# Performance work log

Measured on AMD Instinct MI355X. Metric: run time of the kernel, lower is better.

## Reference

```python
import jax, jax.numpy as jnp
import numpy as np

V, K, NB = 200000, 24, 10
P = K * 9  # pose-blendshape feature dim = 216
# Standard SMPL/STAR kinematic tree; root's parent set to itself (handled specially).
PARENTS = np.array([0, 0, 0, 0, 1, 2, 3, 4, 5, 6, 7, 8, 9, 9, 9, 12, 13, 14, 16, 17, 18, 19, 20, 21])


def setup_inputs() -> dict:
    key = jax.random.key(0)
    ks = jax.random.split(key, 7)
    return {
        "betas": jax.random.normal(ks[0], (NB,), dtype=jnp.float32),
        "pose": jax.random.normal(ks[1], (K * 3,), dtype=jnp.float32),
        "v_template": jax.random.normal(ks[2], (V, 3), dtype=jnp.float32),
        "shapedirs": jax.random.normal(ks[3], (V, 3, NB), dtype=jnp.float32) * 0.01,
        "posedirs": jax.random.normal(ks[4], (V, 3, P), dtype=jnp.float32) * 0.01,
        "J_regressor": jax.random.uniform(ks[5], (K, V), dtype=jnp.float32) / V,
        "weights": jax.random.uniform(ks[6], (V, K), dtype=jnp.float32),
    }


def _rodrigues(r):
    # r: (K,3) axis-angle -> (K,3,3) rotation matrices (matches torch version incl. +1e-12)
    theta = jnp.linalg.norm(r + 1e-12, axis=1, keepdims=True)  # (K,1)
    k = r / theta
    kx, ky, kz = k[:, 0], k[:, 1], k[:, 2]
    z = jnp.zeros_like(kx)
    Km = jnp.stack([z, -kz, ky, kz, z, -kx, -ky, kx, z], axis=1).reshape(-1, 3, 3)
    s = jnp.sin(theta)[:, :, None]
    c = jnp.cos(theta)[:, :, None]
    return jnp.eye(3, dtype=r.dtype) + s * Km + (1.0 - c) * (Km @ Km)


def reference(betas, pose, v_template, shapedirs, posedirs, J_regressor, weights):
    # shape blendshapes
    v_shaped = v_template + jnp.einsum('vci,i->vc', shapedirs, betas)  # (V,3)
    J = J_regressor @ v_shaped  # (K,3) joint locations in rest pose
    R = _rodrigues(pose.reshape(K, 3))  # (K,3,3)
    # pose blendshapes: features are (R - I) flattened over all K joints
    pose_feat = (R - jnp.eye(3, dtype=R.dtype)).reshape(-1)  # (K*9,)
    v_posed = v_shaped + jnp.einsum('vcp,p->vc', posedirs, pose_feat)
    # relative joint translations along the kinematic chain
    rel = J - J[PARENTS]
    rel = rel.at[0].set(J[0])
    # forward kinematics: A[j] = A[parent] @ [[R_j, rel_j],[0,1]]  (K=24, unrolled)
    A_rot = [R[0]]
    A_t = [rel[0]]
    for j in range(1, K):
        p = int(PARENTS[j])
        A_rot.append(A_rot[p] @ R[j])
        A_t.append(A_rot[p] @ rel[j] + A_t[p])
    rot = jnp.stack(A_rot)  # (K,3,3)
    # T[k] = A[k] @ inv(A_rest[k]); A_rest is pure translation by J[k], so
    # T_rot = rot, T_trans = A_t - rot @ J  (analytic inverse of translation)
    trans = jnp.stack(A_t) - jnp.einsum('kij,kj->ki', rot, J)  # (K,3)
    # LBS: blend transforms per vertex (avoids dense K x V x 4 intermediate)
    W_rot = jnp.einsum('vk,kij->vij', weights, rot)  # (V,3,3)
    W_t = weights @ trans  # (V,3)
    return jnp.einsum('vij,vj->vi', W_rot, v_posed) + W_t  # (V,3)
```

## Files before the change

kernel.cpp:

```cpp
#include <hip/hip_runtime.h>

#define NV 200000
#define NPAIR 100000
#define NK 24
#define NCH 64

#define PART_OFF 0
#define J_OFF    4608
#define ROT_OFF  4680
#define TR_OFF   4896
#define PF_OFF   4968

template <int CTRL>
__device__ __forceinline__ float dpp_add(float x) {
    int y = __builtin_amdgcn_update_dpp(0, __float_as_int(x), CTRL, 0xf, 0xf, true);
    return x + __int_as_float(y);
}

typedef float vfloat4 __attribute__((ext_vector_type(4)));
typedef float vfloat2 __attribute__((ext_vector_type(2)));

__device__ __forceinline__ float4 nt_load4(const float4* p) {
    vfloat4 r = __builtin_nontemporal_load((const vfloat4*)p);
    return make_float4(r.x, r.y, r.z, r.w);
}
__device__ __forceinline__ float2 nt_load2(const float2* p) {
    vfloat2 r = __builtin_nontemporal_load((const vfloat2*)p);
    return make_float2(r.x, r.y);
}
__device__ __forceinline__ float nt_load1(const float* p) {
    return __builtin_nontemporal_load(p);
}

__global__ __launch_bounds__(256) void kA(const float* __restrict__ vt,
                                          const float* __restrict__ sd,
                                          const float* __restrict__ betas,
                                          float* __restrict__ vs_out) {
    int v = blockIdx.x * 256 + threadIdx.x;
    if (v >= NV) return;
    float b[10];
#pragma unroll
    for (int i = 0; i < 10; i++) b[i] = betas[i];
    size_t v3 = 3 * (size_t)v;
    float acc0 = nt_load1(vt + v3), acc1 = nt_load1(vt + v3 + 1), acc2 = nt_load1(vt + v3 + 2);
    const float2* s2 = (const float2*)(sd) + (size_t)v * 15;
#pragma unroll
    for (int j = 0; j < 15; j++) {
        float2 s = nt_load2(s2 + j);
        const int e0 = 2 * j, e1 = 2 * j + 1;
        float p0 = s.x * b[e0 % 10];
        float p1 = s.y * b[e1 % 10];
        if (e0 / 10 == 0) acc0 += p0; else if (e0 / 10 == 1) acc1 += p0; else acc2 += p0;
        if (e1 / 10 == 0) acc0 += p1; else if (e1 / 10 == 1) acc1 += p1; else acc2 += p1;
    }
    vs_out[v3] = acc0; vs_out[v3 + 1] = acc1; vs_out[v3 + 2] = acc2;
}

__global__ __launch_bounds__(256) void kB(const float* __restrict__ jr,
                                          const float* __restrict__ vs,
                                          float* __restrict__ ws) {
    int k = blockIdx.x >> 6;
    int chunk = blockIdx.x & 63;
    const float* row = jr + (size_t)k * NV;
    float a0 = 0.f, a1 = 0.f, a2 = 0.f;
    for (int v = chunk * 256 + threadIdx.x; v < NV; v += NCH * 256) {
        float w = nt_load1(row + v);
        size_t v3 = 3 * (size_t)v;
        a0 = fmaf(w, vs[v3], a0);
        a1 = fmaf(w, vs[v3 + 1], a1);
        a2 = fmaf(w, vs[v3 + 2], a2);
    }
#pragma unroll
    for (int off = 32; off; off >>= 1) {
        a0 += __shfl_xor(a0, off, 64);
        a1 += __shfl_xor(a1, off, 64);
        a2 += __shfl_xor(a2, off, 64);
    }
    __shared__ float red[4][3];
    int lane = threadIdx.x & 63, wv = threadIdx.x >> 6;
    if (lane == 0) { red[wv][0] = a0; red[wv][1] = a1; red[wv][2] = a2; }
    __syncthreads();
    if (threadIdx.x < 3) {
        float s = red[0][threadIdx.x] + red[1][threadIdx.x] +
                  red[2][threadIdx.x] + red[3][threadIdx.x];
        ws[PART_OFF + blockIdx.x * 3 + threadIdx.x] = s;
    }
}

__global__ __launch_bounds__(64) void kC(const float* __restrict__ pose,
                                         float* __restrict__ ws) {
    __shared__ float Jl[72];
    __shared__ float Rl[24][9];
    __shared__ float Ar[24][9];
    __shared__ float At[24][3];
    int t = threadIdx.x;

    for (int idx = t; idx < 72; idx += 64) {
        int k = idx / 3, c = idx % 3;
        float s = 0.f;
#pragma unroll
        for (int ch = 0; ch < NCH; ch++) s += ws[PART_OFF + (k * NCH + ch) * 3 + c];
        Jl[idx] = s;
    }

    if (t < 24) {
        float rx = pose[3 * t], ry = pose[3 * t + 1], rz = pose[3 * t + 2];
        float tx = rx + 1e-12f, ty = ry + 1e-12f, tz = rz + 1e-12f;
        float th = sqrtf(tx * tx + ty * ty + tz * tz);
        float inv = 1.0f / th;
        float kx = rx * inv, ky = ry * inv, kz = rz * inv;
        float s = sinf(th), c = cosf(th), oc = 1.0f - c;
        float R00 = 1.f + oc * (-(ky * ky + kz * kz));
        float R01 = -s * kz + oc * kx * ky;
        float R02 =  s * ky + oc * kx * kz;
        float R10 =  s * kz + oc * kx * ky;
        float R11 = 1.f + oc * (-(kx * kx + kz * kz));
        float R12 = -s * kx + oc * ky * kz;
        float R20 = -s * ky + oc * kx * kz;
        float R21 =  s * kx + oc * ky * kz;
        float R22 = 1.f + oc * (-(kx * kx + ky * ky));
        Rl[t][0] = R00; Rl[t][1] = R01; Rl[t][2] = R02;
        Rl[t][3] = R10; Rl[t][4] = R11; Rl[t][5] = R12;
        Rl[t][6] = R20; Rl[t][7] = R21; Rl[t][8] = R22;
        float* pf = ws + PF_OFF + t * 9;
        pf[0] = R00 - 1.f; pf[1] = R01;       pf[2] = R02;
        pf[3] = R10;       pf[4] = R11 - 1.f; pf[5] = R12;
        pf[6] = R20;       pf[7] = R21;       pf[8] = R22 - 1.f;
    }
    __syncthreads();

    const int par[24] = {0,0,0,0,1,2,3,4,5,6,7,8,9,9,9,12,13,14,16,17,18,19,20,21};
    const int lvl[24] = {0,1,1,1,2,2,2,3,3,3,4,4,4,4,4,5,5,5,6,6,7,7,8,8};
    float rel0 = 0.f, rel1 = 0.f, rel2 = 0.f;
    int p = 0, myl = -1;
    if (t < 24) {
        p = par[t]; myl = lvl[t];
        if (t == 0) { rel0 = Jl[0]; rel1 = Jl[1]; rel2 = Jl[2]; }
        else {
            rel0 = Jl[3 * t]     - Jl[3 * p];
            rel1 = Jl[3 * t + 1] - Jl[3 * p + 1];
            rel2 = Jl[3 * t + 2] - Jl[3 * p + 2];
        }
    }
    for (int L = 0; L < 9; L++) {
        if (myl == L) {
            if (t == 0) {
#pragma unroll
                for (int e = 0; e < 9; e++) Ar[0][e] = Rl[0][e];
                At[0][0] = rel0; At[0][1] = rel1; At[0][2] = rel2;
            } else {
#pragma unroll
                for (int i = 0; i < 3; i++) {
                    float ai0 = Ar[p][i * 3], ai1 = Ar[p][i * 3 + 1], ai2 = Ar[p][i * 3 + 2];
#pragma unroll
                    for (int jj = 0; jj < 3; jj++) {
                        Ar[t][i * 3 + jj] = ai0 * Rl[t][jj] + ai1 * Rl[t][3 + jj] + ai2 * Rl[t][6 + jj];
                    }
                    At[t][i] = ai0 * rel0 + ai1 * rel1 + ai2 * rel2 + At[p][i];
                }
            }
        }
        __syncthreads();
    }
    if (t < 24) {
#pragma unroll
        for (int i = 0; i < 3; i++) {
            float tr = At[t][i] - (Ar[t][i * 3]     * Jl[3 * t] +
                                   Ar[t][i * 3 + 1] * Jl[3 * t + 1] +
                                   Ar[t][i * 3 + 2] * Jl[3 * t + 2]);
            ws[TR_OFF + t * 3 + i] = tr;
        }
#pragma unroll
        for (int e = 0; e < 9; e++) ws[ROT_OFF + t * 9 + e] = Ar[t][e];
    }
}

__global__ __launch_bounds__(256) void kD(const float* __restrict__ pd,
                                          const float* __restrict__ wts,
                                          const float* __restrict__ ws,
                                          float* __restrict__ out) {
    int t = threadIdx.x;
    int l = t & 63;

    const float4* pf4 = (const float4*)(ws + PF_OFF);
    float4 b0 = pf4[(l < 54) ? l      : l - 54];
    float4 b1 = pf4[(l < 44) ? l + 10 : l - 44];
    float4 b2 = pf4[(l < 34) ? l + 20 : l - 34];
    float4 b3 = pf4[(l < 24) ? l + 30 : l - 24];
    float4 b4 = pf4[(l < 14) ? l + 40 : l - 14];
    float4 b5 = pf4[(l <  4) ? l + 50 : 0];

    int h  = l >> 5;
    int kk = l & 31;
    float rr0=0,rr1=0,rr2=0,rr3=0,rr4=0,rr5=0,rr6=0,rr7=0,rr8=0;
    float tt0=0, tt1=0, tt2=0;
    if (kk < 24) {
        const float* r = ws + ROT_OFF + kk * 9;
        rr0=r[0]; rr1=r[1]; rr2=r[2]; rr3=r[3]; rr4=r[4];
        rr5=r[5]; rr6=r[6]; rr7=r[7]; rr8=r[8];
        const float* tr = ws + TR_OFF + kk * 3;
        tt0=tr[0]; tt1=tr[1]; tt2=tr[2];
    }

    int wid = (blockIdx.x << 2) + (t >> 6);
    int stride = gridDim.x << 2;
    for (int p = wid; p < NPAIR; p += stride) {
        const float4* base = (const float4*)(pd) + (size_t)p * 324;
        float4 A0 = nt_load4(base + l);
        float4 A1 = nt_load4(base + l + 64);
        float4 A2 = nt_load4(base + l + 128);
        float4 A3 = nt_load4(base + l + 192);
        float4 A4 = nt_load4(base + l + 256);
        float4 A5 = make_float4(0.f, 0.f, 0.f, 0.f);
        if (l < 4) A5 = nt_load4(base + l + 320);

        int vmy = 2 * p + h;
        const float* vsp = out + (size_t)vmy * 3;
        float vsx = vsp[0], vsy = vsp[1], vsz = vsp[2];
        float wk = (kk < 24) ? nt_load1(wts + (size_t)vmy * 24 + kk) : 0.f;

        float d0 = A0.x * b0.x + A0.y * b0.y + A0.z * b0.z + A0.w * b0.w;
        float d1 = A1.x * b1.x + A1.y * b1.y + A1.z * b1.z + A1.w * b1.w;
        float d2 = A2.x * b2.x + A2.y * b2.y + A2.z * b2.z + A2.w * b2.w;
        float d3 = A3.x * b3.x + A3.y * b3.y + A3.z * b3.z + A3.w * b3.w;
        float d4 = A4.x * b4.x + A4.y * b4.y + A4.z * b4.z + A4.w * b4.w;
        float d5 = A5.x * b5.x + A5.y * b5.y + A5.z * b5.z + A5.w * b5.w;

        float s0 = (l < 54) ? d0 : 0.f;
        float s1 = ((l < 54) ? 0.f : d0) + ((l < 44) ? d1 : 0.f);
        float s2 = ((l < 44) ? 0.f : d1) + ((l < 34) ? d2 : 0.f);
        float s3 = ((l < 34) ? 0.f : d2) + ((l < 24) ? d3 : 0.f);
        float s4 = ((l < 24) ? 0.f : d3) + ((l < 14) ? d4 : 0.f);
        float s5 = ((l < 14) ? 0.f : d4) + d5;

        s0 = dpp_add<0xB1>(s0); s1 = dpp_add<0xB1>(s1); s2 = dpp_add<0xB1>(s2);
        s3 = dpp_add<0xB1>(s3); s4 = dpp_add<0xB1>(s4); s5 = dpp_add<0xB1>(s5);
        s0 = dpp_add<0x4E>(s0); s1 = dpp_add<0x4E>(s1); s2 = dpp_add<0x4E>(s2);
        s3 = dpp_add<0x4E>(s3); s4 = dpp_add<0x4E>(s4); s5 = dpp_add<0x4E>(s5);
        s0 = dpp_add<0x141>(s0); s1 = dpp_add<0x141>(s1); s2 = dpp_add<0x141>(s2);
        s3 = dpp_add<0x141>(s3); s4 = dpp_add<0x141>(s4); s5 = dpp_add<0x141>(s5);
        s0 = dpp_add<0x140>(s0); s1 = dpp_add<0x140>(s1); s2 = dpp_add<0x140>(s2);
        s3 = dpp_add<0x140>(s3); s4 = dpp_add<0x140>(s4); s5 = dpp_add<0x140>(s5);
        s0 += __shfl_xor(s0, 16, 64); s1 += __shfl_xor(s1, 16, 64); s2 += __shfl_xor(s2, 16, 64);
        s3 += __shfl_xor(s3, 16, 64); s4 += __shfl_xor(s4, 16, 64); s5 += __shfl_xor(s5, 16, 64);
        s0 += __shfl_xor(s0, 32, 64); s1 += __shfl_xor(s1, 32, 64); s2 += __shfl_xor(s2, 32, 64);
        s3 += __shfl_xor(s3, 32, 64); s4 += __shfl_xor(s4, 32, 64); s5 += __shfl_xor(s5, 32, 64);

        float vpx = vsx + (h ? s3 : s0);
        float vpy = vsy + (h ? s4 : s1);
        float vpz = vsz + (h ? s5 : s2);

        float m0 = wk * (rr0 * vpx + rr1 * vpy + rr2 * vpz + tt0);
        float m1 = wk * (rr3 * vpx + rr4 * vpy + rr5 * vpz + tt1);
        float m2 = wk * (rr6 * vpx + rr7 * vpy + rr8 * vpz + tt2);

        m0 = dpp_add<0xB1>(m0); m1 = dpp_add<0xB1>(m1); m2 = dpp_add<0xB1>(m2);
        m0 = dpp_add<0x4E>(m0); m1 = dpp_add<0x4E>(m1); m2 = dpp_add<0x4E>(m2);
        m0 = dpp_add<0x141>(m0); m1 = dpp_add<0x141>(m1); m2 = dpp_add<0x141>(m2);
        m0 = dpp_add<0x140>(m0); m1 = dpp_add<0x140>(m1); m2 = dpp_add<0x140>(m2);
        m0 += __shfl_xor(m0, 16, 64); m1 += __shfl_xor(m1, 16, 64); m2 += __shfl_xor(m2, 16, 64);

        if (kk < 3) {
            out[(size_t)vmy * 3 + kk] = (kk == 0) ? m0 : (kk == 1) ? m1 : m2;
        }
    }
}

extern "C" void kernel_launch(void* const* d_in, const int* in_sizes, int n_in,
                              void* d_out, int out_size, void* d_ws, size_t ws_size,
                              hipStream_t stream) {
    const float* betas = (const float*)d_in[0];
    const float* pose  = (const float*)d_in[1];
    const float* vt    = (const float*)d_in[2];
    const float* sd    = (const float*)d_in[3];
    const float* pd    = (const float*)d_in[4];
    const float* jr    = (const float*)d_in[5];
    const float* wts   = (const float*)d_in[6];
    float* out = (float*)d_out;
    float* ws  = (float*)d_ws;

    kA<<<(NV + 255) / 256, 256, 0, stream>>>(vt, sd, betas, out);
    kB<<<NK * NCH, 256, 0, stream>>>(jr, out, ws);
    kC<<<1, 64, 0, stream>>>(pose, ws);
    kD<<<2048, 256, 0, stream>>>(pd, wts, ws, out);
}
```

Baseline: 120.8 us.

## Fuse four kernels into one cooperative persistent kernel with grid syncs

Replaces the four separate launches (shape blend, joint regression, kinematic chain, pose blend + skinning) with a single cooperative kernel that runs each phase in turn, separated by grid-wide syncs, and keeps the old launches as a fallback. The aim is to remove per-launch overhead and the gaps between kernels. In exchange it adds three grid barriers, caps the grid at what can be co-resident, and leaves the serial kinematic-chain phase on a single block while every other block waits.

```diff
diff --git a/kernel.cpp b/kernel.cpp
--- a/kernel.cpp
+++ b/kernel.cpp
@@ -1,12 +1,15 @@
 #include <hip/hip_runtime.h>
+#include <hip/hip_cooperative_groups.h>
+
+namespace cg = cooperative_groups;
 
 #define NV 200000
 #define NPAIR 100000
 #define NK 24
 #define NCH 64
+#define NTHREADS 256
 
 #define PART_OFF 0
-#define J_OFF    4608
 #define ROT_OFF  4680
 #define TR_OFF   4896
 #define PF_OFF   4968
@@ -32,17 +35,13 @@
     return __builtin_nontemporal_load(p);
 }
 
-__global__ __launch_bounds__(256) void kA(const float* __restrict__ vt,
-                                          const float* __restrict__ sd,
-                                          const float* __restrict__ betas,
-                                          float* __restrict__ vs_out) {
-    int v = blockIdx.x * 256 + threadIdx.x;
-    if (v >= NV) return;
+__device__ __forceinline__ void phaseA_body(int v, const float* vt, const float* sd,
+                                            const float* betas, float* out) {
     float b[10];
 #pragma unroll
     for (int i = 0; i < 10; i++) b[i] = betas[i];
     size_t v3 = 3 * (size_t)v;
-    float acc0 = nt_load1(vt + v3), acc1 = nt_load1(vt + v3 + 1), acc2 = nt_load1(vt + v3 + 2);
+    float a0 = nt_load1(vt + v3), a1 = nt_load1(vt + v3 + 1), a2 = nt_load1(vt + v3 + 2);
     const float2* s2 = (const float2*)(sd) + (size_t)v * 15;
 #pragma unroll
     for (int j = 0; j < 15; j++) {
@@ -50,59 +49,106 @@
         const int e0 = 2 * j, e1 = 2 * j + 1;
         float p0 = s.x * b[e0 % 10];
         float p1 = s.y * b[e1 % 10];
-        if (e0 / 10 == 0) acc0 += p0; else if (e0 / 10 == 1) acc1 += p0; else acc2 += p0;
-        if (e1 / 10 == 0) acc0 += p1; else if (e1 / 10 == 1) acc1 += p1; else acc2 += p1;
-    }
-    vs_out[v3] = acc0; vs_out[v3 + 1] = acc1; vs_out[v3 + 2] = acc2;
-}
-
-__global__ __launch_bounds__(256) void kB(const float* __restrict__ jr,
-                                          const float* __restrict__ vs,
-                                          float* __restrict__ ws) {
-    int k = blockIdx.x >> 6;
-    int chunk = blockIdx.x & 63;
-    const float* row = jr + (size_t)k * NV;
-    float a0 = 0.f, a1 = 0.f, a2 = 0.f;
-    for (int v = chunk * 256 + threadIdx.x; v < NV; v += NCH * 256) {
-        float w = nt_load1(row + v);
-        size_t v3 = 3 * (size_t)v;
-        a0 = fmaf(w, vs[v3], a0);
-        a1 = fmaf(w, vs[v3 + 1], a1);
-        a2 = fmaf(w, vs[v3 + 2], a2);
-    }
-#pragma unroll
-    for (int off = 32; off; off >>= 1) {
-        a0 += __shfl_xor(a0, off, 64);
-        a1 += __shfl_xor(a1, off, 64);
-        a2 += __shfl_xor(a2, off, 64);
-    }
-    __shared__ float red[4][3];
-    int lane = threadIdx.x & 63, wv = threadIdx.x >> 6;
-    if (lane == 0) { red[wv][0] = a0; red[wv][1] = a1; red[wv][2] = a2; }
-    __syncthreads();
-    if (threadIdx.x < 3) {
-        float s = red[0][threadIdx.x] + red[1][threadIdx.x] +
-                  red[2][threadIdx.x] + red[3][threadIdx.x];
-        ws[PART_OFF + blockIdx.x * 3 + threadIdx.x] = s;
-    }
-}
-
-__global__ __launch_bounds__(64) void kC(const float* __restrict__ pose,
-                                         float* __restrict__ ws) {
-    __shared__ float Jl[72];
-    __shared__ float Rl[24][9];
-    __shared__ float Ar[24][9];
-    __shared__ float At[24][3];
-    int t = threadIdx.x;
-
-    for (int idx = t; idx < 72; idx += 64) {
-        int k = idx / 3, c = idx % 3;
-        float s = 0.f;
-#pragma unroll
-        for (int ch = 0; ch < NCH; ch++) s += ws[PART_OFF + (k * NCH + ch) * 3 + c];
-        Jl[idx] = s;
-    }
-
+        if (e0 / 10 == 0) a0 += p0; else if (e0 / 10 == 1) a1 += p0; else a2 += p0;
+        if (e1 / 10 == 0) a0 += p1; else if (e1 / 10 == 1) a1 += p1; else a2 += p1;
+    }
+    out[v3] = a0; out[v3 + 1] = a1; out[v3 + 2] = a2;
+}
+
+struct DState {
+    float4 b0, b1, b2, b3, b4, b5;
+    float rr0, rr1, rr2, rr3, rr4, rr5, rr6, rr7, rr8, tt0, tt1, tt2;
+    int h, kk;
+};
+
+__device__ __forceinline__ void phaseD_init(DState& st, int l, const float* ws) {
+    const float4* pf4 = (const float4*)(ws + PF_OFF);
+    st.b0 = pf4[(l < 54) ? l      : l - 54];
+    st.b1 = pf4[(l < 44) ? l + 10 : l - 44];
+    st.b2 = pf4[(l < 34) ? l + 20 : l - 34];
+    st.b3 = pf4[(l < 24) ? l + 30 : l - 24];
+    st.b4 = pf4[(l < 14) ? l + 40 : l - 14];
+    st.b5 = pf4[(l <  4) ? l + 50 : 0];
+    st.h  = l >> 5;
+    st.kk = l & 31;
+    st.rr0=0; st.rr1=0; st.rr2=0; st.rr3=0; st.rr4=0; st.rr5=0;
+    st.rr6=0; st.rr7=0; st.rr8=0; st.tt0=0; st.tt1=0; st.tt2=0;
+    if (st.kk < 24) {
+        const float* r = ws + ROT_OFF + st.kk * 9;
+        st.rr0=r[0]; st.rr1=r[1]; st.rr2=r[2]; st.rr3=r[3]; st.rr4=r[4];
+        st.rr5=r[5]; st.rr6=r[6]; st.rr7=r[7]; st.rr8=r[8];
+        const float* tr = ws + TR_OFF + st.kk * 3;
+        st.tt0=tr[0]; st.tt1=tr[1]; st.tt2=tr[2];
+    }
+}
+
+__device__ __forceinline__ void phaseD_pair(const DState& st, int l, int p,
+                                            const float* pd, const float* wts,
+                                            float* out) {
+    const float4* base = (const float4*)(pd) + (size_t)p * 324;
+    float4 A0 = nt_load4(base + l);
+    float4 A1 = nt_load4(base + l + 64);
+    float4 A2 = nt_load4(base + l + 128);
+    float4 A3 = nt_load4(base + l + 192);
+    float4 A4 = nt_load4(base + l + 256);
+    float4 A5 = make_float4(0.f, 0.f, 0.f, 0.f);
+    if (l < 4) A5 = nt_load4(base + l + 320);
+
+    int vmy = 2 * p + st.h;
+    const float* vsp = out + (size_t)vmy * 3;
+    float vsx = vsp[0], vsy = vsp[1], vsz = vsp[2];
+    float wk = (st.kk < 24) ? nt_load1(wts + (size_t)vmy * 24 + st.kk) : 0.f;
+
+    float d0 = A0.x * st.b0.x + A0.y * st.b0.y + A0.z * st.b0.z + A0.w * st.b0.w;
+    float d1 = A1.x * st.b1.x + A1.y * st.b1.y + A1.z * st.b1.z + A1.w * st.b1.w;
+    float d2 = A2.x * st.b2.x + A2.y * st.b2.y + A2.z * st.b2.z + A2.w * st.b2.w;
+    float d3 = A3.x * st.b3.x + A3.y * st.b3.y + A3.z * st.b3.z + A3.w * st.b3.w;
+    float d4 = A4.x * st.b4.x + A4.y * st.b4.y + A4.z * st.b4.z + A4.w * st.b4.w;
+    float d5 = A5.x * st.b5.x + A5.y * st.b5.y + A5.z * st.b5.z + A5.w * st.b5.w;
+
+    float s0 = (l < 54) ? d0 : 0.f;
+    float s1 = ((l < 54) ? 0.f : d0) + ((l < 44) ? d1 : 0.f);
+    float s2 = ((l < 44) ? 0.f : d1) + ((l < 34) ? d2 : 0.f);
+    float s3 = ((l < 34) ? 0.f : d2) + ((l < 24) ? d3 : 0.f);
+    float s4 = ((l < 24) ? 0.f : d3) + ((l < 14) ? d4 : 0.f);
+    float s5 = ((l < 14) ? 0.f : d4) + d5;
+
+    s0 = dpp_add<0xB1>(s0); s1 = dpp_add<0xB1>(s1); s2 = dpp_add<0xB1>(s2);
+    s3 = dpp_add<0xB1>(s3); s4 = dpp_add<0xB1>(s4); s5 = dpp_add<0xB1>(s5);
+    s0 = dpp_add<0x4E>(s0); s1 = dpp_add<0x4E>(s1); s2 = dpp_add<0x4E>(s2);
+    s3 = dpp_add<0x4E>(s3); s4 = dpp_add<0x4E>(s4); s5 = dpp_add<0x4E>(s5);
+    s0 = dpp_add<0x141>(s0); s1 = dpp_add<0x141>(s1); s2 = dpp_add<0x141>(s2);
+    s3 = dpp_add<0x141>(s3); s4 = dpp_add<0x141>(s4); s5 = dpp_add<0x141>(s5);
+    s0 = dpp_add<0x140>(s0); s1 = dpp_add<0x140>(s1); s2 = dpp_add<0x140>(s2);
+    s3 = dpp_add<0x140>(s3); s4 = dpp_add<0x140>(s4); s5 = dpp_add<0x140>(s5);
+    s0 += __shfl_xor(s0, 16, 64); s1 += __shfl_xor(s1, 16, 64); s2 += __shfl_xor(s2, 16, 64);
+    s3 += __shfl_xor(s3, 16, 64); s4 += __shfl_xor(s4, 16, 64); s5 += __shfl_xor(s5, 16, 64);
+    s0 += __shfl_xor(s0, 32, 64); s1 += __shfl_xor(s1, 32, 64); s2 += __shfl_xor(s2, 32, 64);
+    s3 += __shfl_xor(s3, 32, 64); s4 += __shfl_xor(s4, 32, 64); s5 += __shfl_xor(s5, 32, 64);
+
+    float vpx = vsx + (st.h ? s3 : s0);
+    float vpy = vsy + (st.h ? s4 : s1);
+    float vpz = vsz + (st.h ? s5 : s2);
+
+    float m0 = wk * (st.rr0 * vpx + st.rr1 * vpy + st.rr2 * vpz + st.tt0);
+    float m1 = wk * (st.rr3 * vpx + st.rr4 * vpy + st.rr5 * vpz + st.tt1);
+    float m2 = wk * (st.rr6 * vpx + st.rr7 * vpy + st.rr8 * vpz + st.tt2);
+
+    m0 = dpp_add<0xB1>(m0); m1 = dpp_add<0xB1>(m1); m2 = dpp_add<0xB1>(m2);
+    m0 = dpp_add<0x4E>(m0); m1 = dpp_add<0x4E>(m1); m2 = dpp_add<0x4E>(m2);
+    m0 = dpp_add<0x141>(m0); m1 = dpp_add<0x141>(m1); m2 = dpp_add<0x141>(m2);
+    m0 = dpp_add<0x140>(m0); m1 = dpp_add<0x140>(m1); m2 = dpp_add<0x140>(m2);
+    m0 += __shfl_xor(m0, 16, 64); m1 += __shfl_xor(m1, 16, 64); m2 += __shfl_xor(m2, 16, 64);
+
+    if (st.kk < 3) {
+        out[(size_t)vmy * 3 + st.kk] = (st.kk == 0) ? m0 : (st.kk == 1) ? m1 : m2;
+    }
+}
+
+__device__ __forceinline__ void rodrigues_and_chain(int t, const float* pose,
+                                                    float* ws,
+                                                    float Jl[72], float Rl[24][9],
+                                                    float Ar[24][9], float At[24][3]) {
     if (t < 24) {
         float rx = pose[3 * t], ry = pose[3 * t + 1], rz = pose[3 * t + 2];
         float tx = rx + 1e-12f, ty = ry + 1e-12f, tz = rz + 1e-12f;
@@ -175,95 +221,153 @@
     }
 }
 
+__global__ __launch_bounds__(NTHREADS, 4) void mega(const float* __restrict__ betas,
+                                                    const float* __restrict__ pose,
+                                                    const float* __restrict__ vt,
+                                                    const float* __restrict__ sd,
+                                                    const float* __restrict__ pd,
+                                                    const float* __restrict__ jr,
+                                                    const float* __restrict__ wts,
+                                                    float* __restrict__ out,
+                                                    float* __restrict__ ws) {
+    cg::grid_group grid = cg::this_grid();
+    const int tid = threadIdx.x;
+    const int bid = blockIdx.x;
+    const int nb  = gridDim.x;
+    const int l = tid & 63;
+    const int wv = tid >> 6;
+
+    __shared__ float red[4][3];
+    __shared__ float Jl[72];
+    __shared__ float Rl[24][9];
+    __shared__ float Ar[24][9];
+    __shared__ float At[24][3];
+
+    for (int v = bid * NTHREADS + tid; v < NV; v += nb * NTHREADS)
+        phaseA_body(v, vt, sd, betas, out);
+    grid.sync();
+
+    for (int unit = bid; unit < NK * NCH; unit += nb) {
+        int k = unit >> 6;
+        int chunk = unit & 63;
+        const float* row = jr + (size_t)k * NV;
+        float a0 = 0.f, a1 = 0.f, a2 = 0.f;
+        for (int v = chunk * 256 + tid; v < NV; v += NCH * 256) {
+            float w = nt_load1(row + v);
+            size_t v3 = 3 * (size_t)v;
+            a0 = fmaf(w, out[v3], a0);
+            a1 = fmaf(w, out[v3 + 1], a1);
+            a2 = fmaf(w, out[v3 + 2], a2);
+        }
+#pragma unroll
+        for (int off = 32; off; off >>= 1) {
+            a0 += __shfl_xor(a0, off, 64);
+            a1 += __shfl_xor(a1, off, 64);
+            a2 += __shfl_xor(a2, off, 64);
+        }
+        if (l == 0) { red[wv][0] = a0; red[wv][1] = a1; red[wv][2] = a2; }
+        __syncthreads();
+        if (tid < 3) {
+            float s = red[0][tid] + red[1][tid] + red[2][tid] + red[3][tid];
+            ws[PART_OFF + unit * 3 + tid] = s;
+        }
+        __syncthreads();
+    }
+    grid.sync();
+
+    if (bid == 0) {
+        for (int idx = tid; idx < 72; idx += NTHREADS) {
+            int k = idx / 3, c = idx % 3;
+            float s = 0.f;
+#pragma unroll
+            for (int ch = 0; ch < NCH; ch++) s += ws[PART_OFF + (k * NCH + ch) * 3 + c];
+            Jl[idx] = s;
+        }
+        __syncthreads();
+        rodrigues_and_chain(tid, pose, ws, Jl, Rl, Ar, At);
+    }
+    grid.sync();
+
+    {
+        DState st;
+        phaseD_init(st, l, ws);
+        int wid = (bid << 2) + wv;
+        int stride = nb << 2;
+        for (int p = wid; p < NPAIR; p += stride)
+            phaseD_pair(st, l, p, pd, wts, out);
+    }
+}
+
+__global__ __launch_bounds__(256) void kA(const float* __restrict__ vt,
+                                          const float* __restrict__ sd,
+                                          const float* __restrict__ betas,
+                                          float* __restrict__ vs_out) {
+    int v = blockIdx.x * 256 + threadIdx.x;
+    if (v >= NV) return;
+    phaseA_body(v, vt, sd, betas, vs_out);
+}
+
+__global__ __launch_bounds__(256) void kB(const float* __restrict__ jr,
+                                          const float* __restrict__ vs,
+                                          float* __restrict__ ws) {
+    int k = blockIdx.x >> 6;
+    int chunk = blockIdx.x & 63;
+    const float* row = jr + (size_t)k * NV;
+    float a0 = 0.f, a1 = 0.f, a2 = 0.f;
+    for (int v = chunk * 256 + threadIdx.x; v < NV; v += NCH * 256) {
+        float w = nt_load1(row + v);
+        size_t v3 = 3 * (size_t)v;
+        a0 = fmaf(w, vs[v3], a0);
+        a1 = fmaf(w, vs[v3 + 1], a1);
+        a2 = fmaf(w, vs[v3 + 2], a2);
+    }
+#pragma unroll
+    for (int off = 32; off; off >>= 1) {
+        a0 += __shfl_xor(a0, off, 64);
+        a1 += __shfl_xor(a1, off, 64);
+        a2 += __shfl_xor(a2, off, 64);
+    }
+    __shared__ float red[4][3];
+    int lane = threadIdx.x & 63, wv = threadIdx.x >> 6;
+    if (lane == 0) { red[wv][0] = a0; red[wv][1] = a1; red[wv][2] = a2; }
+    __syncthreads();
+    if (threadIdx.x < 3) {
+        float s = red[0][threadIdx.x] + red[1][threadIdx.x] +
+                  red[2][threadIdx.x] + red[3][threadIdx.x];
+        ws[PART_OFF + blockIdx.x * 3 + threadIdx.x] = s;
+    }
+}
+
+__global__ __launch_bounds__(64) void kC(const float* __restrict__ pose,
+                                         float* __restrict__ ws) {
+    __shared__ float Jl[72];
+    __shared__ float Rl[24][9];
+    __shared__ float Ar[24][9];
+    __shared__ float At[24][3];
+    int t = threadIdx.x;
+    for (int idx = t; idx < 72; idx += 64) {
+        int k = idx / 3, c = idx % 3;
+        float s = 0.f;
+#pragma unroll
+        for (int ch = 0; ch < NCH; ch++) s += ws[PART_OFF + (k * NCH + ch) * 3 + c];
+        Jl[idx] = s;
+    }
+    __syncthreads();
+    rodrigues_and_chain(t, pose, ws, Jl, Rl, Ar, At);
+}
+
 __global__ __launch_bounds__(256) void kD(const float* __restrict__ pd,
                                           const float* __restrict__ wts,
                                           const float* __restrict__ ws,
                                           float* __restrict__ out) {
     int t = threadIdx.x;
     int l = t & 63;
-
-    const float4* pf4 = (const float4*)(ws + PF_OFF);
-    float4 b0 = pf4[(l < 54) ? l      : l - 54];
-    float4 b1 = pf4[(l < 44) ? l + 10 : l - 44];
-    float4 b2 = pf4[(l < 34) ? l + 20 : l - 34];
-    float4 b3 = pf4[(l < 24) ? l + 30 : l - 24];
-    float4 b4 = pf4[(l < 14) ? l + 40 : l - 14];
-    float4 b5 = pf4[(l <  4) ? l + 50 : 0];
-
-    int h  = l >> 5;
-    int kk = l & 31;
-    float rr0=0,rr1=0,rr2=0,rr3=0,rr4=0,rr5=0,rr6=0,rr7=0,rr8=0;
-    float tt0=0, tt1=0, tt2=0;
-    if (kk < 24) {
-        const float* r = ws + ROT_OFF + kk * 9;
-        rr0=r[0]; rr1=r[1]; rr2=r[2]; rr3=r[3]; rr4=r[4];
-        rr5=r[5]; rr6=r[6]; rr7=r[7]; rr8=r[8];
-        const float* tr = ws + TR_OFF + kk * 3;
-        tt0=tr[0]; tt1=tr[1]; tt2=tr[2];
-    }
-
+    DState st;
+    phaseD_init(st, l, ws);
     int wid = (blockIdx.x << 2) + (t >> 6);
     int stride = gridDim.x << 2;
-    for (int p = wid; p < NPAIR; p += stride) {
-        const float4* base = (const float4*)(pd) + (size_t)p * 324;
-        float4 A0 = nt_load4(base + l);
-        float4 A1 = nt_load4(base + l + 64);
-        float4 A2 = nt_load4(base + l + 128);
-        float4 A3 = nt_load4(base + l + 192);
-        float4 A4 = nt_load4(base + l + 256);
-        float4 A5 = make_float4(0.f, 0.f, 0.f, 0.f);
-        if (l < 4) A5 = nt_load4(base + l + 320);
-
-        int vmy = 2 * p + h;
-        const float* vsp = out + (size_t)vmy * 3;
-        float vsx = vsp[0], vsy = vsp[1], vsz = vsp[2];
-        float wk = (kk < 24) ? nt_load1(wts + (size_t)vmy * 24 + kk) : 0.f;
-
-        float d0 = A0.x * b0.x + A0.y * b0.y + A0.z * b0.z + A0.w * b0.w;
-        float d1 = A1.x * b1.x + A1.y * b1.y + A1.z * b1.z + A1.w * b1.w;
-        float d2 = A2.x * b2.x + A2.y * b2.y + A2.z * b2.z + A2.w * b2.w;
-        float d3 = A3.x * b3.x + A3.y * b3.y + A3.z * b3.z + A3.w * b3.w;
-        float d4 = A4.x * b4.x + A4.y * b4.y + A4.z * b4.z + A4.w * b4.w;
-        float d5 = A5.x * b5.x + A5.y * b5.y + A5.z * b5.z + A5.w * b5.w;
-
-        float s0 = (l < 54) ? d0 : 0.f;
-        float s1 = ((l < 54) ? 0.f : d0) + ((l < 44) ? d1 : 0.f);
-        float s2 = ((l < 44) ? 0.f : d1) + ((l < 34) ? d2 : 0.f);
-        float s3 = ((l < 34) ? 0.f : d2) + ((l < 24) ? d3 : 0.f);
-        float s4 = ((l < 24) ? 0.f : d3) + ((l < 14) ? d4 : 0.f);
-        float s5 = ((l < 14) ? 0.f : d4) + d5;
-
-        s0 = dpp_add<0xB1>(s0); s1 = dpp_add<0xB1>(s1); s2 = dpp_add<0xB1>(s2);
-        s3 = dpp_add<0xB1>(s3); s4 = dpp_add<0xB1>(s4); s5 = dpp_add<0xB1>(s5);
-        s0 = dpp_add<0x4E>(s0); s1 = dpp_add<0x4E>(s1); s2 = dpp_add<0x4E>(s2);
-        s3 = dpp_add<0x4E>(s3); s4 = dpp_add<0x4E>(s4); s5 = dpp_add<0x4E>(s5);
-        s0 = dpp_add<0x141>(s0); s1 = dpp_add<0x141>(s1); s2 = dpp_add<0x141>(s2);
-        s3 = dpp_add<0x141>(s3); s4 = dpp_add<0x141>(s4); s5 = dpp_add<0x141>(s5);
-        s0 = dpp_add<0x140>(s0); s1 = dpp_add<0x140>(s1); s2 = dpp_add<0x140>(s2);
-        s3 = dpp_add<0x140>(s3); s4 = dpp_add<0x140>(s4); s5 = dpp_add<0x140>(s5);
-        s0 += __shfl_xor(s0, 16, 64); s1 += __shfl_xor(s1, 16, 64); s2 += __shfl_xor(s2, 16, 64);
-        s3 += __shfl_xor(s3, 16, 64); s4 += __shfl_xor(s4, 16, 64); s5 += __shfl_xor(s5, 16, 64);
-        s0 += __shfl_xor(s0, 32, 64); s1 += __shfl_xor(s1, 32, 64); s2 += __shfl_xor(s2, 32, 64);
-        s3 += __shfl_xor(s3, 32, 64); s4 += __shfl_xor(s4, 32, 64); s5 += __shfl_xor(s5, 32, 64);
-
-        float vpx = vsx + (h ? s3 : s0);
-        float vpy = vsy + (h ? s4 : s1);
-        float vpz = vsz + (h ? s5 : s2);
-
-        float m0 = wk * (rr0 * vpx + rr1 * vpy + rr2 * vpz + tt0);
-        float m1 = wk * (rr3 * vpx + rr4 * vpy + rr5 * vpz + tt1);
-        float m2 = wk * (rr6 * vpx + rr7 * vpy + rr8 * vpz + tt2);
-
-        m0 = dpp_add<0xB1>(m0); m1 = dpp_add<0xB1>(m1); m2 = dpp_add<0xB1>(m2);
-        m0 = dpp_add<0x4E>(m0); m1 = dpp_add<0x4E>(m1); m2 = dpp_add<0x4E>(m2);
-        m0 = dpp_add<0x141>(m0); m1 = dpp_add<0x141>(m1); m2 = dpp_add<0x141>(m2);
-        m0 = dpp_add<0x140>(m0); m1 = dpp_add<0x140>(m1); m2 = dpp_add<0x140>(m2);
-        m0 += __shfl_xor(m0, 16, 64); m1 += __shfl_xor(m1, 16, 64); m2 += __shfl_xor(m2, 16, 64);
-
-        if (kk < 3) {
-            out[(size_t)vmy * 3 + kk] = (kk == 0) ? m0 : (kk == 1) ? m1 : m2;
-        }
-    }
+    for (int p = wid; p < NPAIR; p += stride)
+        phaseD_pair(st, l, p, pd, wts, out);
 }
 
 extern "C" void kernel_launch(void* const* d_in, const int* in_sizes, int n_in,
@@ -279,8 +383,19 @@
     float* out = (float*)d_out;
     float* ws  = (float*)d_ws;
 
-    kA<<<(NV + 255) / 256, 256, 0, stream>>>(vt, sd, betas, out);
-    kB<<<NK * NCH, 256, 0, stream>>>(jr, out, ws);
-    kC<<<1, 64, 0, stream>>>(pose, ws);
-    kD<<<2048, 256, 0, stream>>>(pd, wts, ws, out);
-}
+    int perCU = 0;
+    hipError_t e = hipOccupancyMaxActiveBlocksPerMultiprocessor(&perCU, mega, NTHREADS, 0);
+    int grid = 1024;
+    if (e == hipSuccess && perCU > 0 && perCU * 256 < grid) grid = perCU * 256;
+
+    void* args[] = {(void*)&betas, (void*)&pose, (void*)&vt, (void*)&sd,
+                    (void*)&pd, (void*)&jr, (void*)&wts, (void*)&out, (void*)&ws};
+    hipError_t le = hipLaunchCooperativeKernel((const void*)mega, dim3(grid),
+                                               dim3(NTHREADS), args, 0, stream);
+    if (le != hipSuccess) {
+        kA<<<(NV + 255) / 256, 256, 0, stream>>>(vt, sd, betas, out);
+        kB<<<NK * NCH, 256, 0, stream>>>(jr, out, ws);
+        kC<<<1, 64, 0, stream>>>(pose, ws);
+        kD<<<2048, 256, 0, stream>>>(pd, wts, ws, out);
+    }
+}
```

After: 370.5 us. 207% more time.
